# Kernel optimization log

Hardware: AMD Instinct MI355X
Metric: run time of the kernel (lower is better)

The kernel has to match this reference:

```python
import jax, jax.numpy as jnp
import numpy as np

N_NODES = 100000
N_EDGES = 3200000
HIDDEN = 64
OUT = 1


def setup_inputs() -> dict:
    key = jax.random.key(0)
    k_z, k_e, k_w1, k_b1, k_w2, k_b2 = jax.random.split(key, 6)
    z = jax.random.normal(k_z, (N_NODES, HIDDEN), dtype=jnp.float32)
    edge_index = jax.random.randint(k_e, (2, N_EDGES), 0, N_NODES, dtype=jnp.int64)
    # torch Linear default init: U(-1/sqrt(fan_in), 1/sqrt(fan_in))
    lim1 = 1.0 / np.sqrt(2 * HIDDEN)
    lim2 = 1.0 / np.sqrt(HIDDEN)
    W1 = jax.random.uniform(k_w1, (2 * HIDDEN, HIDDEN), jnp.float32, -lim1, lim1)
    b1 = jax.random.uniform(k_b1, (HIDDEN,), jnp.float32, -lim1, lim1)
    W2 = jax.random.uniform(k_w2, (HIDDEN, OUT), jnp.float32, -lim2, lim2)
    b2 = jax.random.uniform(k_b2, (OUT,), jnp.float32, -lim2, lim2)
    return {"z": z, "edge_index": edge_index, "W1": W1, "b1": b1, "W2": W2, "b2": b2}


def reference(z, edge_index, W1, b1, W2, b2):
    row, col = edge_index[0], edge_index[1]
    # gather + concat: [E, 2*HIDDEN]
    h = jnp.concatenate([z[row], z[col]], axis=-1)
    h = jax.nn.relu(h @ W1 + b1)   # [E, HIDDEN]
    out = h @ W2 + b2              # [E, OUT]
    return out
```

## Files before the change

kernel.cpp:

```cpp
#include <hip/hip_runtime.h>
#include <hip/hip_bf16.h>

#define HID 64
#define SST 132

typedef __attribute__((ext_vector_type(8))) short bf16x8;
typedef __attribute__((ext_vector_type(4))) float f32x4;

__device__ __forceinline__ unsigned short f2bf(float f) {
    unsigned int u = __float_as_uint(f);
    return (unsigned short)((u + 0x7fffu + ((u >> 16) & 1u)) >> 16);
}

__device__ __forceinline__ unsigned int pack2bf(float lo, float hi) {
    unsigned int ul = __float_as_uint(lo), uh = __float_as_uint(hi);
    unsigned int rl = (ul + 0x7fffu + ((ul >> 16) & 1u)) >> 16;
    unsigned int rh = (uh + 0x7fffu + ((uh >> 16) & 1u)) & 0xffff0000u;
    return rl | rh;
}

__global__ __launch_bounds__(256) void prep_weights(
    const float* __restrict__ W1, unsigned short* __restrict__ W1bt)
{
    const int t = blockIdx.x * 256 + threadIdx.x;
    const int c = t >> 6, k = t & 63;
    W1bt[t] = f2bf(W1[(((c >> 6) << 6) + k) * HID + (c & 63)]);
}

__global__ __launch_bounds__(256) void node_proj_mfma(
    const float* __restrict__ z, const unsigned short* __restrict__ W1bt,
    const float* __restrict__ b1,
    unsigned short* __restrict__ A, unsigned short* __restrict__ B,
    int n_nodes)
{
    __shared__ alignas(16) unsigned short slds[64 * SST];

    const int t    = threadIdx.x;
    const int lane = t & 63;
    const int wv   = t >> 6;
    const int q    = lane >> 4;
    const int r    = lane & 15;
    const int base = blockIdx.x * 64;

    bf16x8 wf[8][2];
#pragma unroll
    for (int ct = 0; ct < 8; ++ct)
#pragma unroll
        for (int ks = 0; ks < 2; ++ks)
            wf[ct][ks] = *(const bf16x8*)(W1bt + (ct * 16 + r) * HID + ks * 32 + q * 8);

    float bias[4];
#pragma unroll
    for (int i = 0; i < 4; ++i) bias[i] = b1[i * 16 + r];

    const int rowb = base + wv * 16;
    int zrow = rowb + r;
    if (zrow >= n_nodes) zrow = n_nodes - 1;
    const float* zb = z + (size_t)zrow * HID;
    bf16x8 af[2];
#pragma unroll
    for (int ks = 0; ks < 2; ++ks) {
        const float4 f0 = *(const float4*)(zb + ks * 32 + q * 8);
        const float4 f1 = *(const float4*)(zb + ks * 32 + q * 8 + 4);
        unsigned int u[4];
        u[0] = pack2bf(f0.x, f0.y); u[1] = pack2bf(f0.z, f0.w);
        u[2] = pack2bf(f1.x, f1.y); u[3] = pack2bf(f1.z, f1.w);
        af[ks] = *(bf16x8*)u;
    }

#pragma unroll
    for (int ct = 0; ct < 8; ++ct) {
        f32x4 acc = {0.f, 0.f, 0.f, 0.f};
        acc = __builtin_amdgcn_mfma_f32_16x16x32_bf16(af[0], wf[ct][0], acc, 0, 0, 0);
        acc = __builtin_amdgcn_mfma_f32_16x16x32_bf16(af[1], wf[ct][1], acc, 0, 0, 0);
        const float bv = (ct >= 4) ? bias[ct & 3] : 0.0f;
        const int c = ct * 16 + r;
#pragma unroll
        for (int j = 0; j < 4; ++j) {
            const int nl = wv * 16 + q * 4 + j;
            slds[nl * SST + c] = f2bf(acc[j] + bv);
        }
    }
    __syncthreads();

#pragma unroll
    for (int rep = 0; rep < 2; ++rep) {
        const int i   = t + rep * 256;
        const int nl  = i >> 3, seg = i & 7;
        const int ng  = base + nl;
        if (ng < n_nodes) {
            const uint2* pa = (const uint2*)(slds + nl * SST + seg * 8);
            const uint2* pb = (const uint2*)(slds + nl * SST + 64 + seg * 8);
            uint4 va, vb;
            va.x = pa[0].x; va.y = pa[0].y; va.z = pa[1].x; va.w = pa[1].y;
            vb.x = pb[0].x; vb.y = pb[0].y; vb.z = pb[1].x; vb.w = pb[1].y;
            *(uint4*)(A + (size_t)ng * HID + seg * 8) = va;
            *(uint4*)(B + (size_t)ng * HID + seg * 8) = vb;
        }
    }
}

__global__ __launch_bounds__(256) void edge_kernel(
    const int* __restrict__ row, const int* __restrict__ col,
    const unsigned short* __restrict__ A, const unsigned short* __restrict__ B,
    const float* __restrict__ W2, const float* __restrict__ b2,
    float* __restrict__ out, int cbegin, int cend)
{
    const int tid    = blockIdx.x * blockDim.x + threadIdx.x;
    const int lane   = tid & 63;
    const int gwave  = tid >> 6;
    const int nwaves = (gridDim.x * blockDim.x) >> 6;
    const int sub    = lane >> 3;
    const int l8     = lane & 7;

    float w2r[8];
#pragma unroll
    for (int i = 0; i < 8; ++i) w2r[i] = W2[l8 * 8 + i];
    const float b2v = b2[0];

    for (int ch = cbegin + gwave; ch < cend; ch += nwaves) {
        const int ebase = ch << 6;
        const int r = row[ebase + lane];
        const int c = col[ebase + lane];

        uint4 av[8], bv[8];
#pragma unroll
        for (int g = 0; g < 8; ++g) {
            const int ri = __shfl(r, g * 8 + sub);
            const int ci = __shfl(c, g * 8 + sub);
            av[g] = *(const uint4*)(A + (size_t)ri * HID + l8 * 8);
            bv[g] = *(const uint4*)(B + (size_t)ci * HID + l8 * 8);
        }

#pragma unroll
        for (int g = 0; g < 8; ++g) {
            const unsigned int* au = (const unsigned int*)&av[g];
            const unsigned int* bu = (const unsigned int*)&bv[g];
            float acc = 0.f;
#pragma unroll
            for (int i = 0; i < 4; ++i) {
                float alo = __uint_as_float(au[i] << 16);
                float ahi = __uint_as_float(au[i] & 0xffff0000u);
                float blo = __uint_as_float(bu[i] << 16);
                float bhi = __uint_as_float(bu[i] & 0xffff0000u);
                acc = fmaf(fmaxf(alo + blo, 0.f), w2r[2 * i + 0], acc);
                acc = fmaf(fmaxf(ahi + bhi, 0.f), w2r[2 * i + 1], acc);
            }
            acc += __shfl_xor(acc, 4);
            acc += __shfl_xor(acc, 2);
            acc += __shfl_xor(acc, 1);
            if (l8 == 0) out[ebase + g * 8 + sub] = acc + b2v;
        }
    }
}

extern "C" void kernel_launch(void* const* d_in, const int* in_sizes, int n_in,
                              void* d_out, int out_size, void* d_ws, size_t ws_size,
                              hipStream_t stream) {
    const float* z  = (const float*)d_in[0];
    const int*   ei = (const int*)d_in[1];
    const float* W1 = (const float*)d_in[2];
    const float* b1 = (const float*)d_in[3];
    const float* W2 = (const float*)d_in[4];
    const float* b2 = (const float*)d_in[5];
    float* out = (float*)d_out;

    const int n_nodes = in_sizes[0] / HID;
    const int E       = in_sizes[1] / 2;
    const int* row = ei;
    const int* col = ei + E;

    unsigned short* A = (unsigned short*)d_ws;
    unsigned short* B = A + (size_t)n_nodes * HID;
    unsigned short* W1bt = B + (size_t)n_nodes * HID;

    prep_weights<<<32, 256, 0, stream>>>(W1, W1bt);
    const int nblocks = (n_nodes + 63) / 64;
    node_proj_mfma<<<nblocks, 256, 0, stream>>>(z, W1bt, b1, A, B, n_nodes);

    const int nchunks = E >> 6;
    const int half = nchunks / 2;
    edge_kernel<<<2048, 256, 0, stream>>>(row, col, A, B, W2, b2, out, 0, half);
    edge_kernel<<<2048, 256, 0, stream>>>(row, col, A, B, W2, b2, out, half, nchunks);
}
```

Measured before the change: 209.9 us.

## Fold weight prep into node projection and process 64 nodes per wave

Removes the separate prep_weights launch. Each wave now converts W1 to bf16 fragments directly from global memory and reuses them across four 16-node tiles, so each block covers 256 nodes. LDS staging becomes per-wave with an XOR swizzle and 16-byte reads, which removes the block-wide barrier. The edge work split between the two launches also changes from half/half to 2/5 and 3/5. The trade-off is uncoalesced strided W1 reads in every wave and fewer blocks in the projection kernel.

```diff
diff --git a/kernel.cpp b/kernel.cpp
--- a/kernel.cpp
+++ b/kernel.cpp
@@ -2,7 +2,7 @@
 #include <hip/hip_bf16.h>
 
 #define HID 64
-#define SST 132
+#define SST 136
 
 typedef __attribute__((ext_vector_type(8))) short bf16x8;
 typedef __attribute__((ext_vector_type(4))) float f32x4;
@@ -19,83 +19,87 @@
     return rl | rh;
 }
 
-__global__ __launch_bounds__(256) void prep_weights(
-    const float* __restrict__ W1, unsigned short* __restrict__ W1bt)
-{
-    const int t = blockIdx.x * 256 + threadIdx.x;
-    const int c = t >> 6, k = t & 63;
-    W1bt[t] = f2bf(W1[(((c >> 6) << 6) + k) * HID + (c & 63)]);
-}
-
 __global__ __launch_bounds__(256) void node_proj_mfma(
-    const float* __restrict__ z, const unsigned short* __restrict__ W1bt,
+    const float* __restrict__ z, const float* __restrict__ W1,
     const float* __restrict__ b1,
     unsigned short* __restrict__ A, unsigned short* __restrict__ B,
     int n_nodes)
 {
-    __shared__ alignas(16) unsigned short slds[64 * SST];
+    __shared__ alignas(16) unsigned short slds[4 * 16 * SST];
 
     const int t    = threadIdx.x;
     const int lane = t & 63;
     const int wv   = t >> 6;
     const int q    = lane >> 4;
     const int r    = lane & 15;
-    const int base = blockIdx.x * 64;
+    const int gw   = blockIdx.x * 4 + wv;
+
+    unsigned short* __restrict__ sub = slds + wv * 16 * SST;
 
     bf16x8 wf[8][2];
 #pragma unroll
-    for (int ct = 0; ct < 8; ++ct)
+    for (int ct = 0; ct < 8; ++ct) {
+        const int hof = (ct >= 4) ? 64 : 0;
+        const int cw  = (ct & 3) * 16 + r;
 #pragma unroll
-        for (int ks = 0; ks < 2; ++ks)
-            wf[ct][ks] = *(const bf16x8*)(W1bt + (ct * 16 + r) * HID + ks * 32 + q * 8);
+        for (int ks = 0; ks < 2; ++ks) {
+            unsigned short tmp[8];
+#pragma unroll
+            for (int i = 0; i < 8; ++i)
+                tmp[i] = f2bf(W1[(hof + ks * 32 + q * 8 + i) * HID + cw]);
+            wf[ct][ks] = *(bf16x8*)tmp;
+        }
+    }
 
     float bias[4];
 #pragma unroll
     for (int i = 0; i < 4; ++i) bias[i] = b1[i * 16 + r];
 
-    const int rowb = base + wv * 16;
-    int zrow = rowb + r;
-    if (zrow >= n_nodes) zrow = n_nodes - 1;
-    const float* zb = z + (size_t)zrow * HID;
-    bf16x8 af[2];
 #pragma unroll
-    for (int ks = 0; ks < 2; ++ks) {
-        const float4 f0 = *(const float4*)(zb + ks * 32 + q * 8);
-        const float4 f1 = *(const float4*)(zb + ks * 32 + q * 8 + 4);
-        unsigned int u[4];
-        u[0] = pack2bf(f0.x, f0.y); u[1] = pack2bf(f0.z, f0.w);
-        u[2] = pack2bf(f1.x, f1.y); u[3] = pack2bf(f1.z, f1.w);
-        af[ks] = *(bf16x8*)u;
-    }
+    for (int tt = 0; tt < 4; ++tt) {
+        const int rowb = gw * 64 + tt * 16;
+        int zrow = rowb + r;
+        if (zrow >= n_nodes) zrow = n_nodes - 1;
+        const float* zb = z + (size_t)zrow * HID;
+
+        bf16x8 af[2];
+#pragma unroll
+        for (int ks = 0; ks < 2; ++ks) {
+            const float4 f0 = *(const float4*)(zb + ks * 32 + q * 8);
+            const float4 f1 = *(const float4*)(zb + ks * 32 + q * 8 + 4);
+            unsigned int u[4];
+            u[0] = pack2bf(f0.x, f0.y); u[1] = pack2bf(f0.z, f0.w);
+            u[2] = pack2bf(f1.x, f1.y); u[3] = pack2bf(f1.z, f1.w);
+            af[ks] = *(bf16x8*)u;
+        }
 
 #pragma unroll
-    for (int ct = 0; ct < 8; ++ct) {
-        f32x4 acc = {0.f, 0.f, 0.f, 0.f};
-        acc = __builtin_amdgcn_mfma_f32_16x16x32_bf16(af[0], wf[ct][0], acc, 0, 0, 0);
-        acc = __builtin_amdgcn_mfma_f32_16x16x32_bf16(af[1], wf[ct][1], acc, 0, 0, 0);
-        const float bv = (ct >= 4) ? bias[ct & 3] : 0.0f;
-        const int c = ct * 16 + r;
+        for (int ct = 0; ct < 8; ++ct) {
+            f32x4 acc = {0.f, 0.f, 0.f, 0.f};
+            acc = __builtin_amdgcn_mfma_f32_16x16x32_bf16(af[0], wf[ct][0], acc, 0, 0, 0);
+            acc = __builtin_amdgcn_mfma_f32_16x16x32_bf16(af[1], wf[ct][1], acc, 0, 0, 0);
+            const float bv = (ct >= 4) ? bias[ct & 3] : 0.0f;
 #pragma unroll
-        for (int j = 0; j < 4; ++j) {
-            const int nl = wv * 16 + q * 4 + j;
-            slds[nl * SST + c] = f2bf(acc[j] + bv);
+            for (int j = 0; j < 4; ++j) {
+                const int rl = q * 4 + j;
+                const int cx = (ct * 16 + r) ^ ((rl & 8) ? 32 : 0);
+                sub[rl * SST + cx] = f2bf(acc[j] + bv);
+            }
         }
-    }
-    __syncthreads();
 
 #pragma unroll
-    for (int rep = 0; rep < 2; ++rep) {
-        const int i   = t + rep * 256;
-        const int nl  = i >> 3, seg = i & 7;
-        const int ng  = base + nl;
-        if (ng < n_nodes) {
-            const uint2* pa = (const uint2*)(slds + nl * SST + seg * 8);
-            const uint2* pb = (const uint2*)(slds + nl * SST + 64 + seg * 8);
-            uint4 va, vb;
-            va.x = pa[0].x; va.y = pa[0].y; va.z = pa[1].x; va.w = pa[1].y;
-            vb.x = pb[0].x; vb.y = pb[0].y; vb.z = pb[1].x; vb.w = pb[1].y;
-            *(uint4*)(A + (size_t)ng * HID + seg * 8) = va;
-            *(uint4*)(B + (size_t)ng * HID + seg * 8) = vb;
+        for (int p = 0; p < 2; ++p) {
+            const int flat = p * 64 + lane;
+            const int nl   = flat >> 3;
+            const int s    = flat & 7;
+            const int ng   = rowb + nl;
+            const int xr   = (nl & 8) ? 32 : 0;
+            const uint4 va = *(const uint4*)(sub + nl * SST + ((s * 8) ^ xr));
+            const uint4 vb = *(const uint4*)(sub + nl * SST + ((64 + s * 8) ^ xr));
+            if (ng < n_nodes) {
+                *(uint4*)(A + (size_t)ng * HID + s * 8) = va;
+                *(uint4*)(B + (size_t)ng * HID + s * 8) = vb;
+            }
         }
     }
 }
@@ -172,14 +176,12 @@
 
     unsigned short* A = (unsigned short*)d_ws;
     unsigned short* B = A + (size_t)n_nodes * HID;
-    unsigned short* W1bt = B + (size_t)n_nodes * HID;
 
-    prep_weights<<<32, 256, 0, stream>>>(W1, W1bt);
-    const int nblocks = (n_nodes + 63) / 64;
-    node_proj_mfma<<<nblocks, 256, 0, stream>>>(z, W1bt, b1, A, B, n_nodes);
+    const int nblocks = (n_nodes + 255) / 256;
+    node_proj_mfma<<<nblocks, 256, 0, stream>>>(z, W1, b1, A, B, n_nodes);
 
     const int nchunks = E >> 6;
-    const int half = nchunks / 2;
-    edge_kernel<<<2048, 256, 0, stream>>>(row, col, A, B, W2, b2, out, 0, half);
-    edge_kernel<<<2048, 256, 0, stream>>>(row, col, A, B, W2, b2, out, half, nchunks);
+    const int split = (nchunks * 2) / 5;
+    edge_kernel<<<2048, 256, 0, stream>>>(row, col, A, B, W2, b2, out, 0, split);
+    edge_kernel<<<2048, 256, 0, stream>>>(row, col, A, B, W2, b2, out, split, nchunks);
 }
```

Measured after the change: 205.8 us. About the same (-2.0%).
